# Optimization experiments

Hardware: AMD Instinct MI355X
Metric: run time of the kernel (lower is better)

## Reference

```python
import jax, jax.numpy as jnp
import numpy as np

N_NODES = 50000


def _sage_conv(x, src, dst, Wl, Wr, b):
    # PyG SAGEConv (aggr='mean'): out = lin_l(mean_{j in N(i)} x_j) + lin_r(x_i)
    msgs = x[src]                                              # [E, d] gather
    s = jax.ops.segment_sum(msgs, dst, num_segments=N_NODES)   # [N, d]
    cnt = jax.ops.segment_sum(jnp.ones((src.shape[0], 1), x.dtype), dst,
                              num_segments=N_NODES)            # [N, 1]
    agg = s / jnp.maximum(cnt, 1.0)                            # mean, 0 if no nbrs
    return agg @ Wl.T + x @ Wr.T + b


def setup_inputs() -> dict:
    key = jax.random.key(0)
    ks = jax.random.split(key, 12)
    in_dim, h = 128, 128
    E, P = 500000, 200000
    x = jax.random.normal(ks[0], (N_NODES, in_dim), dtype=jnp.float32)
    edge_index = jax.random.randint(ks[1], (2, E), 0, N_NODES)
    pairs = jax.random.randint(ks[2], (P, 2), 0, N_NODES)
    def lin(k, fan_out, fan_in):
        bound = 1.0 / np.sqrt(fan_in)
        return jax.random.uniform(k, (fan_out, fan_in), jnp.float32, -bound, bound)
    return {
        "x": x, "edge_index": edge_index, "pairs": pairs,
        "Wl1": lin(ks[3], h, in_dim), "Wr1": lin(ks[4], h, in_dim),
        "b1": jnp.zeros((h,), jnp.float32),
        "Wl2": lin(ks[5], h, h), "Wr2": lin(ks[6], h, h),
        "b2": jnp.zeros((h,), jnp.float32),
        "W3": lin(ks[7], h, 2 * h), "b3": jnp.zeros((h,), jnp.float32),
        "W4": lin(ks[8], 1, h), "b4": jnp.zeros((1,), jnp.float32),
    }


def reference(x, edge_index, pairs, Wl1, Wr1, b1, Wl2, Wr2, b2, W3, b3, W4, b4):
    src, dst = edge_index[0], edge_index[1]
    h1 = jax.nn.relu(_sage_conv(x, src, dst, Wl1, Wr1, b1))    # [N, h]
    h2 = jax.nn.relu(_sage_conv(h1, src, dst, Wl2, Wr2, b2))   # [N, h]
    a = h2[pairs[:, 0]]                                        # [P, h]
    b = h2[pairs[:, 1]]                                        # [P, h]
    z = jnp.concatenate([a, b], axis=1)                        # [P, 2h]
    s = jax.nn.relu(z @ W3.T + b3) @ W4.T + b4                 # [P, 1]
    return jax.nn.sigmoid(s).squeeze(-1)                       # [P]
```

## Files before the change

### kernel.cpp

```cpp
#include <hip/hip_runtime.h>
#include <math.h>

#define N_NODES 50000
#define E_EDGES 500000
#define P_PAIRS 200000
#define MAX_DEG 64

#define NB        196
#define EB        4096
#define EPT       16
#define SORT_BLKS 123

typedef __bf16    bf16x8 __attribute__((ext_vector_type(8)));
typedef _Float16  f16x8  __attribute__((ext_vector_type(8)));
typedef float     f32x4  __attribute__((ext_vector_type(4)));


#define CONV_BLKS 6250
#define PREP_BLKS 128

__global__ __launch_bounds__(256) void pre_k(
        const float* __restrict__ x, __bf16* __restrict__ xb,
        const int* __restrict__ dst,
        int* __restrict__ bucketCnt, int* __restrict__ blockBase,
        const float* __restrict__ Wl1, const float* __restrict__ Wr1,
        const float* __restrict__ Wl2, const float* __restrict__ Wr2,
        const float* __restrict__ W3,
        __bf16* __restrict__ P1, __bf16* __restrict__ P2, __bf16* __restrict__ P4) {
    __shared__ int cnt[NB];
    int b = blockIdx.x, t = threadIdx.x;
    if (b < SORT_BLKS) {
        if (t < NB) cnt[t] = 0;
        __syncthreads();
        int ebase = b * EB;
        #pragma unroll
        for (int i = 0; i < EPT; ++i) {
            int e = ebase + i * 256 + t;
            if (e < E_EDGES) atomicAdd(&cnt[dst[e] >> 8], 1);
        }
        __syncthreads();
        if (t < NB) blockBase[b * NB + t] = atomicAdd(&bucketCnt[t], cnt[t]);
    } else if (b < SORT_BLKS + CONV_BLKS) {
        int i = (b - SORT_BLKS) * 256 + t;
        float4 v = ((const float4*)x)[i];
        __bf16* o = xb + (size_t)i * 4;
        o[0] = (__bf16)v.x; o[1] = (__bf16)v.y; o[2] = (__bf16)v.z; o[3] = (__bf16)v.w;
    } else {
        int i = (b - SORT_BLKS - CONV_BLKS) * 256 + t;
        int lane = (i >> 3) & 63;
        int j = i & 7;
        int kq = (lane >> 4) * 8 + j;
        {
            int kt = i >> 12, nt = (i >> 9) & 7;
            int n = nt * 16 + (lane & 15);
            int k = kt * 32 + kq;
            P1[i] = (__bf16)((k < 128) ? Wl1[n * 128 + k] : Wr1[n * 128 + (k - 128)]);
            P2[i] = (__bf16)((k < 128) ? Wl2[n * 128 + k] : Wr2[n * 128 + (k - 128)]);
        }
        {
            int kt = i >> 13, nt = (i >> 9) & 15;
            int n = nt * 16 + (lane & 15);
            int k = kt * 32 + kq;
            P4[i] = (__bf16)((n < 128) ? W3[n * 256 + k] : W3[(n - 128) * 256 + 128 + k]);
        }
    }
}


__global__ __launch_bounds__(256) void scan_k(const int* __restrict__ bucketCnt,
                                              int* __restrict__ bucketBase) {
    __shared__ int buf[256];
    int t = threadIdx.x;
    int v = (t < NB) ? bucketCnt[t] : 0;
    buf[t] = v;
    __syncthreads();
    for (int off = 1; off < 256; off <<= 1) {
        int xv = (t >= off) ? buf[t - off] : 0;
        __syncthreads();
        buf[t] += xv;
        __syncthreads();
    }
    if (t < NB) bucketBase[t] = buf[t] - v;
}


__global__ __launch_bounds__(256) void place_k(const int* __restrict__ src,
                                               const int* __restrict__ dst,
                                               const int* __restrict__ bucketBase,
                                               const int* __restrict__ blockBase,
                                               unsigned* __restrict__ edgebuf) {
    __shared__ int cnt[256];
    __shared__ int buf[256];
    __shared__ int sbase[NB];
    __shared__ int gbase[NB];
    __shared__ int cur[NB];
    __shared__ unsigned sortbuf[EB];
    __shared__ unsigned char bktof[EB];
    int blk = blockIdx.x, t = threadIdx.x;
    cnt[t] = 0;
    if (t < NB) cur[t] = 0;
    __syncthreads();

    unsigned packed[EPT];
    int bk[EPT];
    int ebase = blk * EB;
    #pragma unroll
    for (int i = 0; i < EPT; ++i) {
        int e = ebase + i * 256 + t;
        if (e < E_EDGES) {
            int d = dst[e];
            packed[i] = ((unsigned)d << 16) | (unsigned)src[e];
            bk[i] = d >> 8;
            atomicAdd(&cnt[bk[i]], 1);
        } else bk[i] = -1;
    }
    __syncthreads();

    int v = cnt[t];
    buf[t] = v;
    __syncthreads();
    for (int off = 1; off < 256; off <<= 1) {
        int xv = (t >= off) ? buf[t - off] : 0;
        __syncthreads();
        buf[t] += xv;
        __syncthreads();
    }
    if (t < NB) {
        sbase[t] = buf[t] - v;
        gbase[t] = bucketBase[t] + blockBase[blk * NB + t];
    }
    __syncthreads();

    #pragma unroll
    for (int i = 0; i < EPT; ++i) {
        if (bk[i] >= 0) {
            int p = sbase[bk[i]] + atomicAdd(&cur[bk[i]], 1);
            sortbuf[p] = packed[i];
            bktof[p] = (unsigned char)bk[i];
        }
    }
    __syncthreads();

    int nE = E_EDGES - ebase; if (nE > EB) nE = EB;
    for (int i = t; i < nE; i += 256) {
        int bb = bktof[i];
        edgebuf[gbase[bb] + (i - sbase[bb])] = sortbuf[i];
    }
}


__global__ __launch_bounds__(256) void slots_k(const unsigned* __restrict__ edgebuf,
                                               const int* __restrict__ bucketCnt,
                                               const int* __restrict__ bucketBase,
                                               unsigned short* __restrict__ slots,
                                               int* __restrict__ deg) {
    __shared__ unsigned short srow[256 * MAX_DEG];
    __shared__ int cur[256];
    int b = blockIdx.x, t = threadIdx.x;
    cur[t] = 0;
    __syncthreads();
    int base = bucketBase[b], n = bucketCnt[b];
    for (int i = t; i < n; i += 256) {
        unsigned p = edgebuf[base + i];
        int dl = (p >> 16) & 255;
        int pos = atomicAdd(&cur[dl], 1);
        if (pos < MAX_DEG) srow[dl * MAX_DEG + pos] = (unsigned short)(p & 0xFFFFu);
    }
    __syncthreads();
    unsigned* sl32 = (unsigned*)slots;
    const unsigned* sr32 = (const unsigned*)srow;
    int gbase32 = b * 8192;
    for (int i = t; i < 8192; i += 256) {
        int node = b * 256 + (i >> 5);
        if (node < N_NODES) sl32[gbase32 + i] = sr32[i];
    }
    int node = b * 256 + t;
    if (node < N_NODES) deg[node] = cur[t];
}


__global__ __launch_bounds__(256) void agg1_k(const __bf16* __restrict__ feat,
                                              const int* __restrict__ deg_a,
                                              const unsigned short* __restrict__ slots,
                                              __bf16* __restrict__ agg) {
    int n = blockIdx.x * 4 + (threadIdx.x >> 6);
    if (n >= N_NODES) return;
    int lane = threadIdx.x & 63;
    int slot = lane >> 4, l = lane & 15;
    int deg = deg_a[n];
    int nit = (deg < MAX_DEG) ? deg : MAX_DEG;

    int ed = (lane < nit) ? (int)slots[n * MAX_DEG + lane] : 0;

    float s[8];
    #pragma unroll
    for (int e = 0; e < 8; ++e) s[e] = 0.f;

    int trips = (nit + 3) >> 2;
    int it = slot;
    int k = 0;
    for (; k + 1 < trips; k += 2, it += 8) {
        int sn0 = __builtin_amdgcn_ds_bpermute(it << 2, ed);
        int sn1 = __builtin_amdgcn_ds_bpermute((it + 4) << 2, ed);
        bf16x8 v0 = *(const bf16x8*)(feat + (size_t)sn0 * 128 + l * 8);
        bf16x8 v1 = *(const bf16x8*)(feat + (size_t)sn1 * 128 + l * 8);
        if (it < nit) {
            #pragma unroll
            for (int e = 0; e < 8; ++e) s[e] += (float)v0[e];
        }
        if (it + 4 < nit) {
            #pragma unroll
            for (int e = 0; e < 8; ++e) s[e] += (float)v1[e];
        }
    }
    if (k < trips) {
        int sn = __builtin_amdgcn_ds_bpermute(it << 2, ed);
        bf16x8 v = *(const bf16x8*)(feat + (size_t)sn * 128 + l * 8);
        if (it < nit) {
            #pragma unroll
            for (int e = 0; e < 8; ++e) s[e] += (float)v[e];
        }
    }

    #pragma unroll
    for (int e = 0; e < 8; ++e) {
        s[e] += __shfl_xor(s[e], 16, 64);
        s[e] += __shfl_xor(s[e], 32, 64);
    }

    if (slot == 0) {
        float inv = 1.0f / fmaxf((float)deg, 1.0f);
        bf16x8 o;
        #pragma unroll
        for (int e = 0; e < 8; ++e) o[e] = (__bf16)(s[e] * inv);
        *(bf16x8*)(agg + (size_t)n * 128 + l * 8) = o;
    }
}


__global__ __launch_bounds__(256) void layer_mfma_k(const __bf16* __restrict__ agg,
                                                    const __bf16* __restrict__ feat,
                                                    const __bf16* __restrict__ wpack,
                                                    const float* __restrict__ bias,
                                                    __bf16* __restrict__ out) {
    int wave = threadIdx.x >> 6;
    int lane = threadIdx.x & 63;
    int m = lane & 15, quad = lane >> 4;
    int rbase = blockIdx.x * 64 + wave * 16;
    int r0 = rbase + m; if (r0 > N_NODES - 1) r0 = N_NODES - 1;

    f32x4 acc[8];
    #pragma unroll
    for (int nt = 0; nt < 8; ++nt) acc[nt] = (f32x4)0.f;

    #pragma unroll
    for (int kt = 0; kt < 8; ++kt) {
        const __bf16* src = (kt < 4) ? agg : feat;
        int ko = (kt & 3) * 32 + quad * 8;
        bf16x8 a0 = *(const bf16x8*)(src + (size_t)r0 * 128 + ko);
        const __bf16* wb = wpack + (size_t)kt * 4096 + lane * 8;
        #pragma unroll
        for (int nt = 0; nt < 8; ++nt) {
            bf16x8 b = *(const bf16x8*)(wb + nt * 512);
            acc[nt] = __builtin_amdgcn_mfma_f32_16x16x32_bf16(a0, b, acc[nt], 0, 0, 0);
        }
    }

    #pragma unroll
    for (int r = 0; r < 4; ++r) {
        int row = rbase + quad * 4 + r;
        if (row < N_NODES) {
            #pragma unroll
            for (int nt = 0; nt < 8; ++nt) {
                float v = acc[nt][r] + bias[nt * 16 + m];
                out[(size_t)row * 128 + nt * 16 + m] = (__bf16)fmaxf(v, 0.f);
            }
        }
    }
}


__global__ __launch_bounds__(256) void layer2uv_k(const __bf16* __restrict__ agg,
                                                  const __bf16* __restrict__ feat,
                                                  const __bf16* __restrict__ wpack,
                                                  const float* __restrict__ bias,
                                                  const __bf16* __restrict__ wpack4,
                                                  _Float16* __restrict__ UV) {
    __shared__ __bf16 sh[4][16][136];
    int wave = threadIdx.x >> 6;
    int lane = threadIdx.x & 63;
    int m = lane & 15, q = lane >> 4;
    int rbase = blockIdx.x * 64 + wave * 16;
    int r0 = rbase + m; if (r0 > N_NODES - 1) r0 = N_NODES - 1;

    f32x4 acc[8];
    #pragma unroll
    for (int nt = 0; nt < 8; ++nt) acc[nt] = (f32x4)0.f;

    #pragma unroll
    for (int kt = 0; kt < 8; ++kt) {
        const __bf16* src = (kt < 4) ? agg : feat;
        int ko = (kt & 3) * 32 + q * 8;
        bf16x8 a0 = *(const bf16x8*)(src + (size_t)r0 * 128 + ko);
        const __bf16* wb = wpack + (size_t)kt * 4096 + lane * 8;
        #pragma unroll
        for (int nt = 0; nt < 8; ++nt) {
            bf16x8 b = *(const bf16x8*)(wb + nt * 512);
            acc[nt] = __builtin_amdgcn_mfma_f32_16x16x32_bf16(a0, b, acc[nt], 0, 0, 0);
        }
    }

    #pragma unroll
    for (int rr = 0; rr < 4; ++rr)
        #pragma unroll
        for (int nt = 0; nt < 8; ++nt) {
            float v = acc[nt][rr] + bias[nt * 16 + m];
            sh[wave][q * 4 + rr][nt * 16 + m] = (__bf16)fmaxf(v, 0.f);
        }

    f32x4 acc2[16];
    #pragma unroll
    for (int nt = 0; nt < 16; ++nt) acc2[nt] = (f32x4)0.f;

    #pragma unroll
    for (int kt = 0; kt < 4; ++kt) {
        bf16x8 a = *(const bf16x8*)&sh[wave][m][kt * 32 + q * 8];
        const __bf16* wb = wpack4 + (size_t)kt * 8192 + lane * 8;
        #pragma unroll
        for (int nt = 0; nt < 16; ++nt) {
            bf16x8 b = *(const bf16x8*)(wb + nt * 512);
            acc2[nt] = __builtin_amdgcn_mfma_f32_16x16x32_bf16(a, b, acc2[nt], 0, 0, 0);
        }
    }

    #pragma unroll
    for (int rr = 0; rr < 4; ++rr) {
        int row = rbase + q * 4 + rr;
        if (row < N_NODES) {
            #pragma unroll
            for (int nt = 0; nt < 16; ++nt)
                UV[(size_t)row * 256 + nt * 16 + m] = (_Float16)acc2[nt][rr];
        }
    }
}


__global__ __launch_bounds__(256) void pair_ep_k(const _Float16* __restrict__ UV,
                                                 const int* __restrict__ pairs,
                                                 const float* __restrict__ b3,
                                                 const float* __restrict__ W4,
                                                 const float* __restrict__ b4,
                                                 float* __restrict__ out) {
    int t = threadIdx.x;
    int g = t >> 4, l = t & 15;
    int base = blockIdx.x * 64;

    float4 b3a = *(const float4*)(b3 + l * 8);
    float4 b3b = *(const float4*)(b3 + l * 8 + 4);
    float4 w4a = *(const float4*)(W4 + l * 8);
    float4 w4b = *(const float4*)(W4 + l * 8 + 4);
    float bb[8] = {b3a.x, b3a.y, b3a.z, b3a.w, b3b.x, b3b.y, b3b.z, b3b.w};
    float ww[8] = {w4a.x, w4a.y, w4a.z, w4a.w, w4b.x, w4b.y, w4b.z, w4b.w};
    float b4s = b4[0];

    int2 pr[4];
    #pragma unroll
    for (int i = 0; i < 4; ++i) pr[i] = ((const int2*)pairs)[base + i * 16 + g];

    f16x8 ua[4], vb[4];
    #pragma unroll
    for (int i = 0; i < 4; ++i) {
        ua[i] = *(const f16x8*)(UV + (size_t)pr[i].x * 256 + l * 8);
        vb[i] = *(const f16x8*)(UV + (size_t)pr[i].y * 256 + 128 + l * 8);
    }

    #pragma unroll
    for (int i = 0; i < 4; ++i) {
        float p = 0.f;
        #pragma unroll
        for (int e = 0; e < 8; ++e)
            p += fmaxf((float)ua[i][e] + (float)vb[i][e] + bb[e], 0.f) * ww[e];
        #pragma unroll
        for (int s = 1; s < 16; s <<= 1) p += __shfl_xor(p, s, 64);
        if (l == 0)
            out[base + i * 16 + g] = 1.0f / (1.0f + expf(-(p + b4s)));
    }
}


extern "C" void kernel_launch(void* const* d_in, const int* in_sizes, int n_in,
                              void* d_out, int out_size, void* d_ws, size_t ws_size,
                              hipStream_t stream) {
    const float* x   = (const float*)d_in[0];
    const int*   ei  = (const int*)d_in[1];
    const int*   prs = (const int*)d_in[2];
    const float* Wl1 = (const float*)d_in[3];
    const float* Wr1 = (const float*)d_in[4];
    const float* b1  = (const float*)d_in[5];
    const float* Wl2 = (const float*)d_in[6];
    const float* Wr2 = (const float*)d_in[7];
    const float* b2  = (const float*)d_in[8];
    const float* W3  = (const float*)d_in[9];
    const float* b3  = (const float*)d_in[10];
    const float* W4  = (const float*)d_in[11];
    const float* b4  = (const float*)d_in[12];
    float* out = (float*)d_out;

    const int* srcv = ei;
    const int* dstv = ei + E_EDGES;

    char* ws = (char*)d_ws;
    size_t off = 0;
    auto alloc = [&](size_t bytes) -> void* {
        void* p = ws + off;
        off = (off + bytes + 255) & ~(size_t)255;
        return p;
    };
    int*            bucketCnt  = (int*)alloc(sizeof(int) * NB);
    int*            bucketBase = (int*)alloc(sizeof(int) * NB);
    int*            blockBase  = (int*)alloc(sizeof(int) * SORT_BLKS * NB);
    unsigned*       edgebuf    = (unsigned*)alloc(sizeof(unsigned) * E_EDGES);
    int*            deg        = (int*)alloc(sizeof(int) * N_NODES);
    unsigned short* slots      = (unsigned short*)alloc(sizeof(unsigned short) * (size_t)N_NODES * MAX_DEG + 512);
    __bf16*   P1     = (__bf16*)alloc(sizeof(__bf16) * 32768);
    __bf16*   P2     = (__bf16*)alloc(sizeof(__bf16) * 32768);
    __bf16*   P4     = (__bf16*)alloc(sizeof(__bf16) * 32768);
    __bf16*   xb     = (__bf16*)alloc(sizeof(__bf16) * (size_t)N_NODES * 128);
    __bf16*   aggb   = (__bf16*)alloc(sizeof(__bf16) * (size_t)N_NODES * 128);
    __bf16*   h1b    = (__bf16*)alloc(sizeof(__bf16) * (size_t)N_NODES * 128);
    _Float16* UV     = (_Float16*)alloc(sizeof(_Float16) * (size_t)N_NODES * 256);
    (void)ws_size; (void)in_sizes; (void)n_in; (void)out_size;

    hipMemsetAsync(bucketCnt, 0, sizeof(int) * NB, stream);

    pre_k<<<SORT_BLKS + CONV_BLKS + PREP_BLKS, 256, 0, stream>>>(
        x, xb, dstv, bucketCnt, blockBase, Wl1, Wr1, Wl2, Wr2, W3, P1, P2, P4);
    scan_k<<<1, 256, 0, stream>>>(bucketCnt, bucketBase);
    place_k<<<SORT_BLKS, 256, 0, stream>>>(srcv, dstv, bucketBase, blockBase, edgebuf);
    slots_k<<<NB, 256, 0, stream>>>(edgebuf, bucketCnt, bucketBase, slots, deg);

    agg1_k<<<(N_NODES + 3) / 4, 256, 0, stream>>>(xb, deg, slots, aggb);
    layer_mfma_k<<<(N_NODES + 63) / 64, 256, 0, stream>>>(aggb, xb, P1, b1, h1b);
    agg1_k<<<(N_NODES + 3) / 4, 256, 0, stream>>>(h1b, deg, slots, aggb);
    layer2uv_k<<<(N_NODES + 63) / 64, 256, 0, stream>>>(aggb, h1b, P2, b2, P4, UV);
    pair_ep_k<<<P_PAIRS / 64, 256, 0, stream>>>(UV, prs, b3, W4, b4, out);
}
```

Before: 221.9 us.

## Fold bucket scan into place and slots kernels, rebalance sort block sizes

Removes the single-block scan kernel by having each place_k and slots_k block recompute the exclusive prefix sum of the bucket counts redundantly in shared memory, saving one kernel launch and its serialization gap. Sort blocks now each handle 2048 edges instead of 4096, doubling the number of histogram and placement blocks for more parallelism. The x-to-bf16 conversion blocks each process four float4 chunks with a bounds check, so fewer blocks are launched. The trade is redundant scan work and extra barriers in every block, plus a larger blockBase array.

```diff
diff --git a/kernel.cpp b/kernel.cpp
--- a/kernel.cpp
+++ b/kernel.cpp
@@ -7,16 +7,16 @@
 #define MAX_DEG 64
 
 #define NB        196
-#define EB        4096
-#define EPT       16
-#define SORT_BLKS 123
+#define EB        2048
+#define EPT       8
+#define SORT_BLKS 245
 
 typedef __bf16    bf16x8 __attribute__((ext_vector_type(8)));
 typedef _Float16  f16x8  __attribute__((ext_vector_type(8)));
 typedef float     f32x4  __attribute__((ext_vector_type(4)));
 
 
-#define CONV_BLKS 6250
+#define CONV_BLKS 1563
 #define PREP_BLKS 128
 
 __global__ __launch_bounds__(256) void pre_k(
@@ -41,10 +41,16 @@
         __syncthreads();
         if (t < NB) blockBase[b * NB + t] = atomicAdd(&bucketCnt[t], cnt[t]);
     } else if (b < SORT_BLKS + CONV_BLKS) {
-        int i = (b - SORT_BLKS) * 256 + t;
-        float4 v = ((const float4*)x)[i];
-        __bf16* o = xb + (size_t)i * 4;
-        o[0] = (__bf16)v.x; o[1] = (__bf16)v.y; o[2] = (__bf16)v.z; o[3] = (__bf16)v.w;
+        int i0 = (b - SORT_BLKS) * 1024 + t;
+        #pragma unroll
+        for (int k = 0; k < 4; ++k) {
+            int i = i0 + k * 256;
+            if (i < N_NODES * 128 / 4) {
+                float4 v = ((const float4*)x)[i];
+                __bf16* o = xb + (size_t)i * 4;
+                o[0] = (__bf16)v.x; o[1] = (__bf16)v.y; o[2] = (__bf16)v.z; o[3] = (__bf16)v.w;
+            }
+        }
     } else {
         int i = (b - SORT_BLKS - CONV_BLKS) * 256 + t;
         int lane = (i >> 3) & 63;
@@ -67,26 +73,9 @@
 }
 
 
-__global__ __launch_bounds__(256) void scan_k(const int* __restrict__ bucketCnt,
-                                              int* __restrict__ bucketBase) {
-    __shared__ int buf[256];
-    int t = threadIdx.x;
-    int v = (t < NB) ? bucketCnt[t] : 0;
-    buf[t] = v;
-    __syncthreads();
-    for (int off = 1; off < 256; off <<= 1) {
-        int xv = (t >= off) ? buf[t - off] : 0;
-        __syncthreads();
-        buf[t] += xv;
-        __syncthreads();
-    }
-    if (t < NB) bucketBase[t] = buf[t] - v;
-}
-
-
 __global__ __launch_bounds__(256) void place_k(const int* __restrict__ src,
                                                const int* __restrict__ dst,
-                                               const int* __restrict__ bucketBase,
+                                               const int* __restrict__ bucketCnt,
                                                const int* __restrict__ blockBase,
                                                unsigned* __restrict__ edgebuf) {
     __shared__ int cnt[256];
@@ -97,6 +86,17 @@
     __shared__ unsigned sortbuf[EB];
     __shared__ unsigned char bktof[EB];
     int blk = blockIdx.x, t = threadIdx.x;
+
+    int bv = (t < NB) ? bucketCnt[t] : 0;
+    buf[t] = bv;
+    __syncthreads();
+    for (int off = 1; off < 256; off <<= 1) {
+        int xv = (t >= off) ? buf[t - off] : 0;
+        __syncthreads();
+        buf[t] += xv;
+        __syncthreads();
+    }
+    if (t < NB) gbase[t] = (buf[t] - bv) + blockBase[blk * NB + t];
     cnt[t] = 0;
     if (t < NB) cur[t] = 0;
     __syncthreads();
@@ -125,10 +125,7 @@
         buf[t] += xv;
         __syncthreads();
     }
-    if (t < NB) {
-        sbase[t] = buf[t] - v;
-        gbase[t] = bucketBase[t] + blockBase[blk * NB + t];
-    }
+    if (t < NB) sbase[t] = buf[t] - v;
     __syncthreads();
 
     #pragma unroll
@@ -151,15 +148,28 @@
 
 __global__ __launch_bounds__(256) void slots_k(const unsigned* __restrict__ edgebuf,
                                                const int* __restrict__ bucketCnt,
-                                               const int* __restrict__ bucketBase,
                                                unsigned short* __restrict__ slots,
                                                int* __restrict__ deg) {
     __shared__ unsigned short srow[256 * MAX_DEG];
     __shared__ int cur[256];
+    __shared__ int buf[256];
+    __shared__ int sc[2];
     int b = blockIdx.x, t = threadIdx.x;
+
+    int bv = (t < NB) ? bucketCnt[t] : 0;
+    buf[t] = bv;
     cur[t] = 0;
     __syncthreads();
-    int base = bucketBase[b], n = bucketCnt[b];
+    for (int off = 1; off < 256; off <<= 1) {
+        int xv = (t >= off) ? buf[t - off] : 0;
+        __syncthreads();
+        buf[t] += xv;
+        __syncthreads();
+    }
+    if (t == b) { sc[0] = buf[t] - bv; sc[1] = bv; }
+    __syncthreads();
+    int base = sc[0], n = sc[1];
+
     for (int i = t; i < n; i += 256) {
         unsigned p = edgebuf[base + i];
         int dl = (p >> 16) & 255;
@@ -417,7 +427,6 @@
         return p;
     };
     int*            bucketCnt  = (int*)alloc(sizeof(int) * NB);
-    int*            bucketBase = (int*)alloc(sizeof(int) * NB);
     int*            blockBase  = (int*)alloc(sizeof(int) * SORT_BLKS * NB);
     unsigned*       edgebuf    = (unsigned*)alloc(sizeof(unsigned) * E_EDGES);
     int*            deg        = (int*)alloc(sizeof(int) * N_NODES);
@@ -435,9 +444,8 @@
 
     pre_k<<<SORT_BLKS + CONV_BLKS + PREP_BLKS, 256, 0, stream>>>(
         x, xb, dstv, bucketCnt, blockBase, Wl1, Wr1, Wl2, Wr2, W3, P1, P2, P4);
-    scan_k<<<1, 256, 0, stream>>>(bucketCnt, bucketBase);
-    place_k<<<SORT_BLKS, 256, 0, stream>>>(srcv, dstv, bucketBase, blockBase, edgebuf);
-    slots_k<<<NB, 256, 0, stream>>>(edgebuf, bucketCnt, bucketBase, slots, deg);
+    place_k<<<SORT_BLKS, 256, 0, stream>>>(srcv, dstv, bucketCnt, blockBase, edgebuf);
+    slots_k<<<NB, 256, 0, stream>>>(edgebuf, bucketCnt, slots, deg);
 
     agg1_k<<<(N_NODES + 3) / 4, 256, 0, stream>>>(xb, deg, slots, aggb);
     layer_mfma_k<<<(N_NODES + 63) / 64, 256, 0, stream>>>(aggb, xb, P1, b1, h1b);
```

Result: faster. 217.0 us (-2.2%).
